# Optimization experiments

Measured on AMD Instinct MI355X. Metric: run time of the kernel, lower is better.

## Reference

```python
import jax, jax.numpy as jnp
import numpy as np

N_QUBITS = 12
N_LAYERS = 4
BATCH = 4096
DIM = 2 ** N_QUBITS  # 4096


def _apply_1q(state, U, q):
    """Apply 2x2 complex gate U to qubit q. state: (B,) + (2,)*n, wire 0 = MSB (axis q+1)."""
    state = jnp.moveaxis(state, q + 1, -1)
    state = state @ U.T
    return jnp.moveaxis(state, -1, q + 1)


def _apply_cnot(state, c, t):
    """CNOT with control c, target t: flip target amplitudes where control bit == 1."""
    flipped = jnp.flip(state, axis=t + 1)
    shape = [2 if i == c + 1 else 1 for i in range(state.ndim)]
    ctrl = jnp.arange(2).reshape(shape)
    return jnp.where(ctrl == 1, flipped, state)


def setup_inputs() -> dict:
    key = jax.random.key(0)
    k1, k2 = jax.random.split(key)
    x = jax.random.normal(k1, (BATCH, DIM), dtype=jnp.float32)
    weights = jax.random.normal(k2, (N_LAYERS, N_QUBITS, 2), dtype=jnp.float32) * 0.1
    return {"x": x, "weights": weights}


def reference(x, weights):
    n, L = N_QUBITS, N_LAYERS
    B = x.shape[0]
    # AmplitudeEmbedding with normalize=True
    norm = jnp.linalg.norm(x, axis=-1, keepdims=True)
    state = (x / norm).astype(jnp.complex64).reshape((B,) + (2,) * n)
    for layer in range(L):
        for q in range(n):
            ty = weights[layer, q, 0]
            tz = weights[layer, q, 1]
            c, s = jnp.cos(ty / 2), jnp.sin(ty / 2)
            em = jnp.exp(-0.5j * tz.astype(jnp.complex64))  # e^{-i tz/2}
            ep = jnp.exp(+0.5j * tz.astype(jnp.complex64))
            # U = RZ(tz) @ RY(ty), fused single 2x2 gate per qubit
            U = jnp.stack([
                jnp.stack([c * em, -s * em]),
                jnp.stack([s * ep, c * ep]),
            ]).astype(jnp.complex64)
            state = _apply_1q(state, U, q)
        for q in range(n - 1):
            state = _apply_cnot(state, q, q + 1)
        if n > 2:
            state = _apply_cnot(state, n - 1, 0)
    probs = jnp.abs(state) ** 2  # (B,) + (2,)*n, float32
    reduce_axes = tuple(range(1, probs.ndim))
    outs = []
    for q in range(n):
        shape = [2 if i == q + 1 else 1 for i in range(probs.ndim)]
        sign = jnp.array([1.0, -1.0], dtype=probs.dtype).reshape(shape)
        outs.append(jnp.sum(probs * sign, axis=reduce_axes))
    return jnp.stack(outs, axis=-1)  # (B, n_qubits) <Z_q> expvals
```

## Files before the change

### kernel.cpp

```cpp
#include <hip/hip_runtime.h>

#define NQ   12
#define DIM  4096
#define NL   4
#define BLK  256

typedef unsigned short u16;
typedef unsigned int   u32;

struct L12 { u16 b[NQ]; };

static constexpr u32 lap(const L12& A, u32 x){ u32 r=0; for(int p=0;p<NQ;++p) if((x>>p)&1u) r^=A.b[p]; return r; }
static constexpr L12 lcomp(const L12& A, const L12& B){ L12 r{}; for(int p=0;p<NQ;++p) r.b[p]=(u16)lap(A,(u32)B.b[p]); return r; }
static constexpr L12 lident(){ L12 r{}; for(int p=0;p<NQ;++p) r.b[p]=(u16)(1u<<p); return r; }

static constexpr u32 applyT(u32 i){
  i ^= ((i>>0)&1u) << 11;
  for(int q=10;q>=0;--q){ int pc=11-q, pt=10-q; i ^= ((i>>pc)&1u) << pt; }
  return i;
}
static constexpr L12 lT(){ L12 t{}; for(int p=0;p<NQ;++p) t.b[p]=(u16)applyT(1u<<p); return t; }

static constexpr L12 linv(const L12& A){
  u16 v[NQ]; u16 u[NQ];
  for(int p=0;p<NQ;++p){ v[p]=A.b[p]; u[p]=(u16)(1u<<p); }
  for(int t=0;t<NQ;++t){
    int p=t; while(!((v[p]>>t)&1u)) ++p;
    u16 tv=v[p]; v[p]=v[t]; v[t]=tv; u16 tu=u[p]; u[p]=u[t]; u[t]=tu;
    for(int k=0;k<NQ;++k) if(k!=t && ((v[k]>>t)&1u)){ v[k]^=v[t]; u[k]^=u[t]; }
  }
  L12 r{}; for(int p=0;p<NQ;++p) r.b[p]=u[p]; return r;
}
static constexpr L12 ltr(const L12& A){
  L12 r{}; for(int p=0;p<NQ;++p) for(int q=0;q<NQ;++q) if((A.b[p]>>q)&1u) r.b[q]=(u16)(r.b[q]|(1u<<p));
  return r;
}
static constexpr int cpop(u32 v){ int n=0; while(v){ n+=(int)(v&1u); v>>=1; } return n; }

struct Tables {
  u16 cm[12][16];
  u16 wg[12][4];
  u16 sp[12][4];
  u16 wexp[NQ];
};

static constexpr Tables make_tables(){
  Tables tb{};
  const L12 T   = lT();
  const L12 Tit = ltr(linv(T));
  L12 A = lident();
  L12 W = lident();
  for(int l=0;l<NL;++l){
    for(int g=0;g<3;++g){
      const int st = l*3+g;
      u16 mm[4]={0,0,0,0};
      for(int i=0;i<4;++i){ mm[i]=A.b[4*g+i]; tb.wg[st][i]=W.b[4*g+i]; }
      u32 ech[4]={0,0,0,0}; int piv[4]={0,0,0,0};
      for(int i=0;i<4;++i){
        u32 v=mm[i];
        for(int k=0;k<i;++k) if((v>>piv[k])&1u) v^=ech[k];
        int t2=11; while(!((v>>t2)&1u)) --t2;
        piv[i]=t2; ech[i]=v;
      }
      for(int a2=0;a2<4;++a2) for(int b2=a2+1;b2<4;++b2)
        if(piv[b2]<piv[a2]){ int tt=piv[a2]; piv[a2]=piv[b2]; piv[b2]=tt; }
      for(int i=0;i<4;++i) tb.sp[st][i]=(u16)piv[i];
      for(int c=0;c<16;++c){ u32 m=0; for(int i=0;i<4;++i) if((c>>i)&1) m^=mm[i]; tb.cm[st][c]=(u16)m; }
    }
    A = lcomp(A, T);
    W = lcomp(W, Tit);
  }
  for(int p=0;p<NQ;++p) tb.wexp[p]=W.b[p];
  return tb;
}

__device__ constexpr Tables TB = make_tables();

static constexpr u16 UIMG[12] = {1,2,4,8, 3,5,6,7, 9,10,11,13};

static constexpr u32 swz(u32 j){
  u32 f=0;
  for(int k=4;k<12;++k) if((j>>k)&1u) f ^= (u32)UIMG[k];
  return j ^ (f & 15u);
}

struct Derived {
  u32 lane_c[12][8];
  u32 smb[12][4];
  u32 scmb[12][16];
  u32 g0lane[8];
  u32 u11lane[8];
  u32 u11smb[4];
  u16 csgn[12];
  u16 pm[12];
};

static constexpr Derived make_derived(){
  const Tables tb = make_tables();
  Derived d{};
  for(int st=0; st<12; ++st){
    bool isp[12]={false,false,false,false,false,false,false,false,false,false,false,false};
    for(int i=0;i<4;++i) isp[tb.sp[st][i]]=true;
    int np[8]; int nn=0;
    for(int p=0;p<12;++p) if(!isp[p]) np[nn++]=p;
    int best=-1;
    for(int ms=0; ms<256; ++ms){
      int pc=0; for(int k=0;k<8;++k) pc+=(ms>>k)&1;
      if(pc!=6) continue;
      u16 bas[4]={0,0,0,0}; int r=0;
      for(int k=0;k<8;++k){
        if(!((ms>>k)&1)) continue;
        u16 x=(u16)(UIMG[np[k]]&15);
        while(x){
          int hb=3; while(!((x>>hb)&1)) --hb;
          if(bas[hb]) x=(u16)(x^bas[hb]);
          else { bas[hb]=x; ++r; x=0; }
        }
      }
      if(r==4){ best=ms; break; }
    }
    if(best<0) best=0x3F;
    int pos[8]; int lo=0, hi=6;
    for(int k=0;k<8;++k){ if((best>>k)&1) pos[lo++]=np[k]; else pos[hi++]=np[k]; }
    for(int k=0;k<8;++k){
      const u32 addr = swz(1u<<pos[k])<<3;
      u32 nib=0;
      for(int i=0;i<4;++i) nib |= (u32)((tb.wg[st][i]>>pos[k])&1u)<<i;
      d.lane_c[st][k] = addr | (nib<<28);
      if(st==0)  d.g0lane[k]  = 1u<<pos[k];
      if(st==11) d.u11lane[k] = 1u<<pos[k];
    }
    for(int i=0;i<4;++i)  d.smb[st][i]  = swz((u32)tb.cm[st][1<<i])<<3;
    for(int c=0;c<16;++c) d.scmb[st][c] = swz((u32)tb.cm[st][c])<<3;
    if(st==11) for(int i=0;i<4;++i) d.u11smb[i] = (u32)tb.cm[11][1<<i];
  }
  for(int q=0;q<12;++q){
    d.pm[q] = tb.wexp[11-q];
    u16 m=0;
    for(int c=0;c<16;++c){
      const int par = cpop((u32)tb.cm[11][c] & (u32)tb.wexp[11-q]) & 1;
      m |= (u16)(par<<c);
    }
    d.csgn[q]=m;
  }
  return d;
}

__device__ constexpr Derived DV = make_derived();

template<int ST, bool WITHW>
__device__ __forceinline__ void gates(float (&ar)[16], float (&ai)[16], const float4* __restrict__ gw){
#pragma unroll
  for(int i=0;i<4;++i){
    const float4 g = gw[ST*4+i];
#pragma unroll
    for(int c=0;c<16;++c){
      if((c>>i)&1) continue;
      const int c1 = c|(1<<i);
      float ur = fmaf(-g.x, ar[c1], ar[c]);
      float ui = fmaf(-g.x, ai[c1], ai[c]);
      float vr = fmaf( g.y, ur, ar[c1]);
      float vi = fmaf( g.y, ui, ai[c1]);
      ar[c] = fmaf(-g.x, vr, ur);
      ai[c] = fmaf(-g.x, vi, ui);
      if(WITHW){
        const float t = fmaf(-g.z, vi, vr);
        vi = fmaf( g.w, t, vi);
        vr = fmaf(-g.z, vi, t);
      }
      ar[c1]=vr; ai[c1]=vi;
    }
  }
}

template<int ST, bool WITHW>
__device__ __forceinline__ void mid_step(const u32* msk, char* lds, const float4* __restrict__ gw){
  u32 acc=0;
#pragma unroll
  for(int k=0;k<8;++k) acc ^= DV.lane_c[ST][k]&msk[k];
  const u32 nib = acc>>28;
  u32 base = acc & 0x0FFFFFFFu;
#pragma unroll
  for(int i=0;i<4;++i) base ^= DV.smb[ST][i] & (0u-((nib>>i)&1u));
  u32 ad[16]; float ar[16], ai[16];
#pragma unroll
  for(int c=0;c<16;++c){
    ad[c] = base ^ DV.scmb[ST][c];
    const float2 v = *(const float2*)(lds+ad[c]);
    ar[c]=v.x; ai[c]=v.y;
  }
  gates<ST,WITHW>(ar,ai,gw);
#pragma unroll
  for(int c=0;c<16;++c){ float2 v; v.x=ar[c]; v.y=ai[c]; *(float2*)(lds+ad[c])=v; }
  __syncthreads();
}

__global__ void prep_kernel(const float* __restrict__ w, float4* __restrict__ gw){
  const int t = threadIdx.x;
  if(t < NL*NQ){
    const int l=t/NQ, p=t%NQ, q=(NQ-1)-p;
    const float ty=w[(l*NQ+q)*2+0], tz=w[(l*NQ+q)*2+1];
    gw[t]=make_float4(tanf(0.25f*ty), sinf(0.5f*ty), tanf(0.5f*tz), sinf(tz));
  }
}

__global__ __launch_bounds__(BLK, 4) void qsim_kernel(const float* __restrict__ x,
                                                      const float4* __restrict__ gw,
                                                      float* __restrict__ out)
{
  __shared__ float2 st2[DIM];
  __shared__ float  wred[4][13];
  char* lds = (char*)st2;
  const int tid = threadIdx.x;
  const int bb  = blockIdx.x;

  u32 msk[8];
#pragma unroll
  for(int k=0;k<8;++k) msk[k]=0u-((u32)(tid>>k)&1u);

  u32 rep0=0, acc0=0;
#pragma unroll
  for(int k=0;k<8;++k){ rep0 ^= DV.g0lane[k]&msk[k]; acc0 ^= DV.lane_c[0][k]&msk[k]; }
  const u32 base0 = acc0 & 0x0FFFFFFFu;

  float ar[16], ai[16];
  const float* xr = x + (size_t)bb*DIM + rep0;
#pragma unroll
  for(int s=0;s<4;++s){
    const float4 v = *reinterpret_cast<const float4*>(xr + 4*s);
    ar[4*s+0]=v.x; ar[4*s+1]=v.y; ar[4*s+2]=v.z; ar[4*s+3]=v.w;
    ai[4*s+0]=0.f; ai[4*s+1]=0.f; ai[4*s+2]=0.f; ai[4*s+3]=0.f;
  }
  gates<0,true>(ar,ai,gw);
#pragma unroll
  for(int c=0;c<16;++c){ float2 v; v.x=ar[c]; v.y=ai[c];
    *(float2*)(lds + (base0 ^ DV.scmb[0][c])) = v; }
  __syncthreads();

  mid_step<1,true >(msk,lds,gw);
  mid_step<2,true >(msk,lds,gw);
  mid_step<3,true >(msk,lds,gw);
  mid_step<4,true >(msk,lds,gw);
  mid_step<5,true >(msk,lds,gw);
  mid_step<6,true >(msk,lds,gw);
  mid_step<7,true >(msk,lds,gw);
  mid_step<8,true >(msk,lds,gw);
  mid_step<9,false>(msk,lds,gw);
  mid_step<10,false>(msk,lds,gw);

  {
    u32 acc=0, urep=0;
#pragma unroll
    for(int k=0;k<8;++k){ acc ^= DV.lane_c[11][k]&msk[k]; urep ^= DV.u11lane[k]&msk[k]; }
    const u32 nib = acc>>28;
    u32 base = acc & 0x0FFFFFFFu;
#pragma unroll
    for(int i=0;i<4;++i){ const u32 mi=0u-((nib>>i)&1u); base ^= DV.smb[11][i]&mi; urep ^= DV.u11smb[i]&mi; }
#pragma unroll
    for(int c=0;c<16;++c){
      const float2 v = *(const float2*)(lds + (base ^ DV.scmb[11][c]));
      ar[c]=v.x; ai[c]=v.y;
    }
    gates<11,false>(ar,ai,gw);

    float pr[16]; float nrm=0.f;
#pragma unroll
    for(int c=0;c<16;++c) pr[c]=fmaf(ar[c],ar[c], ai[c]*ai[c]);
#pragma unroll
    for(int c=0;c<16;++c) nrm += pr[c];
    float accq[12];
#pragma unroll
    for(int q=0;q<12;++q){
      float a=0.f;
#pragma unroll
      for(int c=0;c<16;++c){ if((DV.csgn[q]>>c)&1) a-=pr[c]; else a+=pr[c]; }
      const u32 sb = ((u32)__popc(urep & (u32)DV.pm[q]) & 1u)<<31;
      accq[q]=__uint_as_float(__float_as_uint(a)^sb);
    }
#pragma unroll
    for(int o=32;o;o>>=1){
      nrm += __shfl_xor(nrm,o);
#pragma unroll
      for(int q=0;q<12;++q) accq[q]+=__shfl_xor(accq[q],o);
    }
    const int wid=tid>>6;
    if((tid&63)==0){
#pragma unroll
      for(int q=0;q<12;++q) wred[wid][q]=accq[q];
      wred[wid][12]=nrm;
    }
    __syncthreads();
    if(tid<NQ){
      const float s0=wred[0][tid]+wred[1][tid]+wred[2][tid]+wred[3][tid];
      const float sn=wred[0][12]+wred[1][12]+wred[2][12]+wred[3][12];
      out[(size_t)bb*NQ+tid]=s0/sn;
    }
  }
}

extern "C" void kernel_launch(void* const* d_in, const int* in_sizes, int n_in,
                              void* d_out, int out_size, void* d_ws, size_t ws_size,
                              hipStream_t stream) {
  const float* x = (const float*)d_in[0];
  const float* w = (const float*)d_in[1];
  float* out = (float*)d_out;
  float4* gw = (float4*)d_ws;
  const int B = in_sizes[0] / DIM;
  prep_kernel<<<1, 64, 0, stream>>>(w, gw);
  qsim_kernel<<<B, BLK, 0, stream>>>(x, gw, out);
}
```

Baseline: 112.7 us.

## Pack complex amplitudes as float2 vectors, use Walsh-Hadamard for expvals, raise occupancy

Amplitudes are held as 2-wide float vectors so the gate FMAs can lower to packed FP32 instructions on CDNA. The final per-qubit sign sums are replaced by an in-register Walsh-Hadamard transform, and each expval is then picked by a precomputed index. The reduction scratch reuses the state LDS buffer, with an extra barrier, instead of its own shared array. The launch bound goes from 4 to 5 blocks per SM, which caps registers and could cause spills.

```diff
diff --git a/kernel.cpp b/kernel.cpp
--- a/kernel.cpp
+++ b/kernel.cpp
@@ -7,6 +7,7 @@
 
 typedef unsigned short u16;
 typedef unsigned int   u32;
+typedef float f2 __attribute__((ext_vector_type(2)));
 
 struct L12 { u16 b[NQ]; };
 
@@ -91,8 +92,8 @@
   u32 g0lane[8];
   u32 u11lane[8];
   u32 u11smb[4];
-  u16 csgn[12];
   u16 pm[12];
+  u16 mu[12];
 };
 
 static constexpr Derived make_derived(){
@@ -136,12 +137,9 @@
   }
   for(int q=0;q<12;++q){
     d.pm[q] = tb.wexp[11-q];
-    u16 m=0;
-    for(int c=0;c<16;++c){
-      const int par = cpop((u32)tb.cm[11][c] & (u32)tb.wexp[11-q]) & 1;
-      m |= (u16)(par<<c);
-    }
-    d.csgn[q]=m;
+    u32 m=0;
+    for(int i=0;i<4;++i) m |= (u32)(cpop((u32)tb.cm[11][1u<<i] & (u32)tb.wexp[11-q])&1)<<i;
+    d.mu[q]=(u16)m;
   }
   return d;
 }
@@ -149,26 +147,25 @@
 __device__ constexpr Derived DV = make_derived();
 
 template<int ST, bool WITHW>
-__device__ __forceinline__ void gates(float (&ar)[16], float (&ai)[16], const float4* __restrict__ gw){
+__device__ __forceinline__ void gates(f2 (&a)[16], const float4* __restrict__ gw){
 #pragma unroll
   for(int i=0;i<4;++i){
     const float4 g = gw[ST*4+i];
+    const f2 mt = {-g.x, -g.x};
+    const f2 sy = { g.y,  g.y};
 #pragma unroll
     for(int c=0;c<16;++c){
       if((c>>i)&1) continue;
       const int c1 = c|(1<<i);
-      float ur = fmaf(-g.x, ar[c1], ar[c]);
-      float ui = fmaf(-g.x, ai[c1], ai[c]);
-      float vr = fmaf( g.y, ur, ar[c1]);
-      float vi = fmaf( g.y, ui, ai[c1]);
-      ar[c] = fmaf(-g.x, vr, ur);
-      ai[c] = fmaf(-g.x, vi, ui);
+      f2 u = __builtin_elementwise_fma(mt, a[c1], a[c]);
+      f2 v = __builtin_elementwise_fma(sy, u, a[c1]);
+      a[c] = __builtin_elementwise_fma(mt, v, u);
       if(WITHW){
-        const float t = fmaf(-g.z, vi, vr);
-        vi = fmaf( g.w, t, vi);
-        vr = fmaf(-g.z, vi, t);
+        const float t = fmaf(-g.z, v.y, v.x);
+        v.y = fmaf( g.w, t, v.y);
+        v.x = fmaf(-g.z, v.y, t);
       }
-      ar[c1]=vr; ai[c1]=vi;
+      a[c1]=v;
     }
   }
 }
@@ -182,16 +179,15 @@
   u32 base = acc & 0x0FFFFFFFu;
 #pragma unroll
   for(int i=0;i<4;++i) base ^= DV.smb[ST][i] & (0u-((nib>>i)&1u));
-  u32 ad[16]; float ar[16], ai[16];
+  u32 ad[16]; f2 a[16];
 #pragma unroll
   for(int c=0;c<16;++c){
     ad[c] = base ^ DV.scmb[ST][c];
-    const float2 v = *(const float2*)(lds+ad[c]);
-    ar[c]=v.x; ai[c]=v.y;
-  }
-  gates<ST,WITHW>(ar,ai,gw);
-#pragma unroll
-  for(int c=0;c<16;++c){ float2 v; v.x=ar[c]; v.y=ai[c]; *(float2*)(lds+ad[c])=v; }
+    a[c] = *(const f2*)(lds+ad[c]);
+  }
+  gates<ST,WITHW>(a,gw);
+#pragma unroll
+  for(int c=0;c<16;++c){ *(f2*)(lds+ad[c]) = a[c]; }
   __syncthreads();
 }
 
@@ -204,12 +200,11 @@
   }
 }
 
-__global__ __launch_bounds__(BLK, 4) void qsim_kernel(const float* __restrict__ x,
+__global__ __launch_bounds__(BLK, 5) void qsim_kernel(const float* __restrict__ x,
                                                       const float4* __restrict__ gw,
                                                       float* __restrict__ out)
 {
-  __shared__ float2 st2[DIM];
-  __shared__ float  wred[4][13];
+  __shared__ f2 st2[DIM];
   char* lds = (char*)st2;
   const int tid = threadIdx.x;
   const int bb  = blockIdx.x;
@@ -223,18 +218,17 @@
   for(int k=0;k<8;++k){ rep0 ^= DV.g0lane[k]&msk[k]; acc0 ^= DV.lane_c[0][k]&msk[k]; }
   const u32 base0 = acc0 & 0x0FFFFFFFu;
 
-  float ar[16], ai[16];
+  f2 a[16];
   const float* xr = x + (size_t)bb*DIM + rep0;
 #pragma unroll
   for(int s=0;s<4;++s){
     const float4 v = *reinterpret_cast<const float4*>(xr + 4*s);
-    ar[4*s+0]=v.x; ar[4*s+1]=v.y; ar[4*s+2]=v.z; ar[4*s+3]=v.w;
-    ai[4*s+0]=0.f; ai[4*s+1]=0.f; ai[4*s+2]=0.f; ai[4*s+3]=0.f;
-  }
-  gates<0,true>(ar,ai,gw);
-#pragma unroll
-  for(int c=0;c<16;++c){ float2 v; v.x=ar[c]; v.y=ai[c];
-    *(float2*)(lds + (base0 ^ DV.scmb[0][c])) = v; }
+    a[4*s+0]=(f2){v.x,0.f}; a[4*s+1]=(f2){v.y,0.f};
+    a[4*s+2]=(f2){v.z,0.f}; a[4*s+3]=(f2){v.w,0.f};
+  }
+  gates<0,true>(a,gw);
+#pragma unroll
+  for(int c=0;c<16;++c){ *(f2*)(lds + (base0 ^ DV.scmb[0][c])) = a[c]; }
   __syncthreads();
 
   mid_step<1,true >(msk,lds,gw);
@@ -258,41 +252,47 @@
     for(int i=0;i<4;++i){ const u32 mi=0u-((nib>>i)&1u); base ^= DV.smb[11][i]&mi; urep ^= DV.u11smb[i]&mi; }
 #pragma unroll
     for(int c=0;c<16;++c){
-      const float2 v = *(const float2*)(lds + (base ^ DV.scmb[11][c]));
-      ar[c]=v.x; ai[c]=v.y;
-    }
-    gates<11,false>(ar,ai,gw);
-
-    float pr[16]; float nrm=0.f;
-#pragma unroll
-    for(int c=0;c<16;++c) pr[c]=fmaf(ar[c],ar[c], ai[c]*ai[c]);
-#pragma unroll
-    for(int c=0;c<16;++c) nrm += pr[c];
+      a[c] = *(const f2*)(lds + (base ^ DV.scmb[11][c]));
+    }
+    gates<11,false>(a,gw);
+
+    float pr[16];
+#pragma unroll
+    for(int c=0;c<16;++c) pr[c]=fmaf(a[c].x,a[c].x, a[c].y*a[c].y);
+#pragma unroll
+    for(int b=1;b<16;b<<=1){
+#pragma unroll
+      for(int c=0;c<16;++c){
+        if(c&b) continue;
+        const float u=pr[c], v=pr[c|b];
+        pr[c]=u+v; pr[c|b]=u-v;
+      }
+    }
     float accq[12];
 #pragma unroll
     for(int q=0;q<12;++q){
-      float a=0.f;
-#pragma unroll
-      for(int c=0;c<16;++c){ if((DV.csgn[q]>>c)&1) a-=pr[c]; else a+=pr[c]; }
       const u32 sb = ((u32)__popc(urep & (u32)DV.pm[q]) & 1u)<<31;
-      accq[q]=__uint_as_float(__float_as_uint(a)^sb);
-    }
+      accq[q]=__uint_as_float(__float_as_uint(pr[DV.mu[q]])^sb);
+    }
+    float nrm2 = pr[0];
 #pragma unroll
     for(int o=32;o;o>>=1){
-      nrm += __shfl_xor(nrm,o);
+      nrm2 += __shfl_xor(nrm2,o);
 #pragma unroll
       for(int q=0;q<12;++q) accq[q]+=__shfl_xor(accq[q],o);
     }
+    __syncthreads();
+    float* wredf = (float*)lds;
     const int wid=tid>>6;
     if((tid&63)==0){
 #pragma unroll
-      for(int q=0;q<12;++q) wred[wid][q]=accq[q];
-      wred[wid][12]=nrm;
+      for(int q=0;q<12;++q) wredf[wid*13+q]=accq[q];
+      wredf[wid*13+12]=nrm2;
     }
     __syncthreads();
     if(tid<NQ){
-      const float s0=wred[0][tid]+wred[1][tid]+wred[2][tid]+wred[3][tid];
-      const float sn=wred[0][12]+wred[1][12]+wred[2][12]+wred[3][12];
+      const float s0=wredf[0*13+tid]+wredf[1*13+tid]+wredf[2*13+tid]+wredf[3*13+tid];
+      const float sn=wredf[0*13+12]+wredf[1*13+12]+wredf[2*13+12]+wredf[3*13+12];
       out[(size_t)bb*NQ+tid]=s0/sn;
     }
   }
```

Result: faster. 107.0 us (-5.1%).
